# Kernel tuning notes

Measured on AMD Instinct MI355X. Metric: run time of the kernel, lower is better.

Reference implementation:

```python
import jax, jax.numpy as jnp
import numpy as np

N = 50000
E = 800000
D_IN, D_HID, D_OUT = 256, 256, 128


def _xavier(key, shape):
    fan_in, fan_out = shape
    limit = float(np.sqrt(6.0 / (fan_in + fan_out)))
    return jax.random.uniform(key, shape, jnp.float32, -limit, limit)


def setup_inputs() -> dict:
    key = jax.random.key(0)
    ks = jax.random.split(key, 12)
    x = jax.random.normal(ks[0], (N, D_IN), jnp.float32)
    edge_index = jax.random.randint(ks[1], (2, E), 0, N, dtype=jnp.int64)
    batch = jnp.zeros((N,), jnp.int64)
    # per-layer: message weight W, linear weight LW (stored [in, out]), bias b
    w1 = _xavier(ks[2], (D_IN, D_HID))
    lw1 = _xavier(ks[3], (D_IN, D_HID))
    lb1 = jnp.zeros((D_HID,), jnp.float32)
    w2 = _xavier(ks[4], (D_HID, D_HID))
    lw2 = _xavier(ks[5], (D_HID, D_HID))
    lb2 = jnp.zeros((D_HID,), jnp.float32)
    w3 = _xavier(ks[6], (D_HID, D_OUT))
    lw3 = _xavier(ks[7], (D_HID, D_OUT))
    lb3 = jnp.zeros((D_OUT,), jnp.float32)
    return {"x": x, "edge_index": edge_index, "batch": batch,
            "w1": w1, "lw1": lw1, "lb1": lb1,
            "w2": w2, "lw2": lw2, "lb2": lb2,
            "w3": w3, "lw3": lw3, "lb3": lb3}


def _gcn_layer(x, W, LW, b, row, col, norm):
    # message: norm * (x_j @ W); equivalent and cheaper: transform nodes once, gather
    xw = x @ W                                   # [N, out]
    msg = norm[:, None] * xw[row]                # [E, out]
    agg = jax.ops.segment_sum(msg, col, num_segments=x.shape[0])  # scatter-add at col
    return agg + x @ LW + b                      # residual linear path


def reference(x, edge_index, batch, w1, lw1, lb1, w2, lw2, lb2, w3, lw3, lb3):
    row, col = edge_index[0], edge_index[1]
    ones = jnp.ones((row.shape[0],), x.dtype)
    out_deg = jax.ops.segment_sum(ones, row, num_segments=N)
    in_deg = jax.ops.segment_sum(ones, col, num_segments=N)
    # inf at zero-degree nodes never gets gathered (those nodes have no edges)
    norm = out_deg[row] ** -0.5 * in_deg[col] ** -0.5  # [E]

    h = jax.nn.relu(_gcn_layer(x, w1, lw1, lb1, row, col, norm))
    h = jax.nn.relu(_gcn_layer(h, w2, lw2, lb2, row, col, norm))
    h = jax.nn.sigmoid(_gcn_layer(h, w3, lw3, lb3, row, col, norm))
    return h
```

## Files before the change

kernel.cpp:

```cpp
#include <hip/hip_runtime.h>
#include <hip/hip_bf16.h>
#include <math.h>

#define NNODES 50000
#define NEDGES 800000
#define HNB 128
#define HBINS 50176
#define SCAN_NB 196

typedef short s8v __attribute__((ext_vector_type(8)));
typedef float f4v __attribute__((ext_vector_type(4)));
using bf16 = __hip_bfloat16;

static __device__ __forceinline__ float bflo(unsigned int x) {
    union { unsigned int i; float f; } c; c.i = x << 16; return c.f;
}
static __device__ __forceinline__ float bfhi(unsigned int x) {
    union { unsigned int i; float f; } c; c.i = x & 0xffff0000u; return c.f;
}

static __device__ __forceinline__ void gload16(const void* g, void* l) {
    __builtin_amdgcn_global_load_lds(
        (const __attribute__((address_space(1))) unsigned int*)g,
        (__attribute__((address_space(3))) unsigned int*)l, 16, 0, 0);
}


__global__ void k_packbt(const float* __restrict__ W, const float* __restrict__ LW,
                         bf16* __restrict__ out, int K, int C) {
    int i = blockIdx.x * blockDim.x + threadIdx.x;
    int C2 = 2 * C;
    if (i >= K * C2) return;
    int n = i / K, k = i % K;
    float v = (n < C) ? W[k * C + n] : LW[k * C + (n - C)];
    out[i] = __float2bfloat16(v);
}


__global__ __launch_bounds__(256) void k_hist(const int* __restrict__ ei, ushort* __restrict__ partials) {
    __shared__ unsigned int h32[HBINS / 2];
    int b = blockIdx.x, row = blockIdx.y, t = threadIdx.x;
    for (int i = t; i < HBINS / 2; i += 256) h32[i] = 0;
    __syncthreads();
    const int chunk = NEDGES / HNB;
    int beg = b * chunk, end = beg + chunk;
    const int* p = ei + (size_t)row * NEDGES;
    for (int e = beg + t; e < end; e += 256) {
        int id = p[e];
        atomicAdd(&h32[id >> 1], 1u << (16 * (id & 1)));
    }
    __syncthreads();
    unsigned int* o32 = (unsigned int*)(partials + ((size_t)row * HNB + b) * HBINS);
    for (int i = t; i < HBINS / 2; i += 256) o32[i] = h32[i];
}

__global__ __launch_bounds__(256) void k_hist_reduce(const ushort* __restrict__ partials,
                                                     float* __restrict__ rsqrt_out,
                                                     int* __restrict__ in_cnt,
                                                     int* __restrict__ block_sums) {
    __shared__ int sm[256];
    int row = blockIdx.y;
    int i = blockIdx.x * 256 + threadIdx.x;
    const ushort* p = partials + (size_t)row * HNB * HBINS + i;
    int s = 0;
#pragma unroll 4
    for (int b = 0; b < HNB; ++b) s += p[(size_t)b * HBINS];
    if (row == 0) {
        if (i < NNODES) rsqrt_out[i] = rsqrtf((float)s);
    } else {
        if (i < NNODES) in_cnt[i] = s;
        sm[threadIdx.x] = s;
        __syncthreads();
        for (int off = 128; off > 0; off >>= 1) {
            if (threadIdx.x < off) sm[threadIdx.x] += sm[threadIdx.x + off];
            __syncthreads();
        }
        if (threadIdx.x == 0) block_sums[blockIdx.x] = sm[0];
    }
}


__global__ void k_scan_blocks(const int* __restrict__ block_sums, int* __restrict__ block_base, int nb) {
    __shared__ int s[256];
    int t = threadIdx.x;
    int v = (t < nb) ? block_sums[t] : 0;
    s[t] = v;
    __syncthreads();
    for (int off = 1; off < 256; off <<= 1) {
        int u = (t >= off) ? s[t - off] : 0;
        __syncthreads();
        s[t] += u;
        __syncthreads();
    }
    block_base[t] = s[t] - v;
}

__global__ void k_scan_final(const int* __restrict__ in_cnt, const int* __restrict__ block_base,
                             int* __restrict__ offsets, int* __restrict__ cursor) {
    __shared__ int s[256];
    int b = blockIdx.x, t = threadIdx.x;
    int i = b * 256 + t;
    int v = (i < NNODES) ? in_cnt[i] : 0;
    s[t] = v;
    __syncthreads();
    for (int off = 1; off < 256; off <<= 1) {
        int u = (t >= off) ? s[t - off] : 0;
        __syncthreads();
        s[t] += u;
        __syncthreads();
    }
    int excl = s[t] - v + block_base[b];
    if (i < NNODES) { offsets[i] = excl; cursor[i] = excl; }
    if (i == NNODES - 1) offsets[NNODES] = excl + v;
}

__global__ void k_scatter(const int* __restrict__ ei, int* __restrict__ cursor,
                          int* __restrict__ src_sorted) {
    int e = blockIdx.x * blockDim.x + threadIdx.x;
    if (e < NEDGES) {
        int r = ei[e], c = ei[NEDGES + e];
        int p = atomicAdd(&cursor[c], 1);
        src_sorted[p] = r;
    }
}

template<int D, int C2, int ACT>
__global__ __launch_bounds__(64) void k_agg_fused(const bf16* __restrict__ xwcat,
                                                  const int* __restrict__ offsets,
                                                  const int* __restrict__ src_sorted,
                                                  const float* __restrict__ rsqrt_out,
                                                  const float* __restrict__ bias,
                                                  void* __restrict__ out) {
    const int L = D / 8;
    const int G = 64 / L;
    const int U = 4;
    int lane = threadIdx.x;
    int v = blockIdx.x;
    int g = lane / L, sl = lane % L;

    int beg = offsets[v], end = offsets[v + 1];
    int deg = end - beg;
    int dcap = min(deg, 64);

    int id = 0; float wl = 0.f;
    if (lane < dcap) {
        id = src_sorted[beg + lane];
        wl = rsqrt_out[id];
    }

    float acc[U][8];
#pragma unroll
    for (int u = 0; u < U; ++u)
#pragma unroll
        for (int c = 0; c < 8; ++c) acc[u][c] = 0.f;

    const ushort* base = (const ushort*)xwcat + sl * 8;

    for (int e0 = 0; e0 < dcap; e0 += G * U) {
#pragma unroll
        for (int u = 0; u < U; ++u) {
            int e = e0 + u * G + g;
            int s = __shfl(id, e & 63, 64);
            float w = __shfl(wl, e & 63, 64);
            if (e >= dcap) w = 0.f;
            uint4 q = *(const uint4*)(base + (size_t)s * C2);
            acc[u][0] += w * bflo(q.x); acc[u][1] += w * bfhi(q.x);
            acc[u][2] += w * bflo(q.y); acc[u][3] += w * bfhi(q.y);
            acc[u][4] += w * bflo(q.z); acc[u][5] += w * bfhi(q.z);
            acc[u][6] += w * bflo(q.w); acc[u][7] += w * bfhi(q.w);
        }
    }
    for (int j = beg + 64 + g; j < end; j += G) {
        int s = src_sorted[j];
        float w = rsqrt_out[s];
        uint4 q = *(const uint4*)(base + (size_t)s * C2);
        acc[0][0] += w * bflo(q.x); acc[0][1] += w * bfhi(q.x);
        acc[0][2] += w * bflo(q.y); acc[0][3] += w * bfhi(q.y);
        acc[0][4] += w * bflo(q.z); acc[0][5] += w * bfhi(q.z);
        acc[0][6] += w * bflo(q.w); acc[0][7] += w * bfhi(q.w);
    }

#pragma unroll
    for (int c = 0; c < 8; ++c) acc[0][c] = (acc[0][c] + acc[1][c]) + (acc[2][c] + acc[3][c]);
#pragma unroll
    for (int d = 32; d >= L; d >>= 1) {
#pragma unroll
        for (int c = 0; c < 8; ++c) acc[0][c] += __shfl_down(acc[0][c], d, 64);
    }

    if (lane < L) {
        float sc = (deg > 0) ? rsqrtf((float)deg) : 0.f;
        const ushort* lwp = (const ushort*)xwcat + (size_t)v * C2 + D + sl * 8;
        uint4 ql = *(const uint4*)lwp;
        const float* bp = bias + sl * 8;
        float4 b0 = *(const float4*)bp, b1 = *(const float4*)(bp + 4);
        float h[8];
        h[0] = acc[0][0] * sc + bflo(ql.x) + b0.x;
        h[1] = acc[0][1] * sc + bfhi(ql.x) + b0.y;
        h[2] = acc[0][2] * sc + bflo(ql.y) + b0.z;
        h[3] = acc[0][3] * sc + bfhi(ql.y) + b0.w;
        h[4] = acc[0][4] * sc + bflo(ql.z) + b1.x;
        h[5] = acc[0][5] * sc + bfhi(ql.z) + b1.y;
        h[6] = acc[0][6] * sc + bflo(ql.w) + b1.z;
        h[7] = acc[0][7] * sc + bfhi(ql.w) + b1.w;
        if (ACT == 1) {
            union { bf16 hh[8]; uint4 u; } o;
#pragma unroll
            for (int c = 0; c < 8; ++c) o.hh[c] = __float2bfloat16(fmaxf(h[c], 0.f));
            *(uint4*)((ushort*)out + (size_t)v * D + sl * 8) = o.u;
        } else {
            float r[8];
#pragma unroll
            for (int c = 0; c < 8; ++c) r[c] = 1.f / (1.f + expf(-h[c]));
            float* op = (float*)out + (size_t)v * D + sl * 8;
            *(float4*)op = (float4){r[0], r[1], r[2], r[3]};
            *(float4*)(op + 4) = (float4){r[4], r[5], r[6], r[7]};
        }
    }
}

template<int C2, bool A_BF16>
__global__ __launch_bounds__(256) void k_gemm2(const void* __restrict__ Aptr,
                                               const bf16* __restrict__ BT,
                                               bf16* __restrict__ Out) {
    constexpr int R = NNODES;
    constexpr int GX = (NNODES + 127) / 128;
    constexpr int GY = C2 / 128;
    constexpr int NWG = GX * GY;
    __shared__ bf16 As[128 * 32];
    __shared__ bf16 Bs[128 * 32];

    int o = blockIdx.x;
    constexpr int qq = NWG / 8, rr = NWG % 8;
    int xcd = o & 7, idx = o >> 3;
    int lt = (xcd < rr ? xcd * (qq + 1) : rr * (qq + 1) + (xcd - rr) * qq) + idx;
    int r0 = (lt / GY) * 128;
    int n0 = (lt % GY) * 128;

    int t = threadIdx.x;
    int wave = t >> 6, lane = t & 63;
    int wr = wave >> 1, wc = wave & 1;

    f4v acc[4][4];
#pragma unroll
    for (int mi = 0; mi < 4; ++mi)
#pragma unroll
        for (int ni = 0; ni < 4; ++ni) acc[mi][ni] = (f4v){0.f, 0.f, 0.f, 0.f};

    int sr = t >> 2;
    int sk = (t & 3) * 8;
    int fr = t >> 1, fs = (t & 1) * 16;

    for (int k0 = 0; k0 < 256; k0 += 32) {
        if (A_BF16) {
            const bf16* Ab = (const bf16*)Aptr;
            gload16(Ab + (size_t)min(r0 + sr, R - 1) * 256 + k0 + sk,
                    (char*)As + wave * 1024);
            gload16(Ab + (size_t)min(r0 + sr + 64, R - 1) * 256 + k0 + sk,
                    (char*)As + 4096 + wave * 1024);
        } else {
            const float* Af = (const float*)Aptr + (size_t)min(r0 + fr, R - 1) * 256 + k0 + fs;
            float4 f0 = ((const float4*)Af)[0];
            float4 f1 = ((const float4*)Af)[1];
            float4 f2 = ((const float4*)Af)[2];
            float4 f3 = ((const float4*)Af)[3];
            union { bf16 h[16]; uint4 u[2]; } cv;
            cv.h[0]  = __float2bfloat16(f0.x); cv.h[1]  = __float2bfloat16(f0.y);
            cv.h[2]  = __float2bfloat16(f0.z); cv.h[3]  = __float2bfloat16(f0.w);
            cv.h[4]  = __float2bfloat16(f1.x); cv.h[5]  = __float2bfloat16(f1.y);
            cv.h[6]  = __float2bfloat16(f1.z); cv.h[7]  = __float2bfloat16(f1.w);
            cv.h[8]  = __float2bfloat16(f2.x); cv.h[9]  = __float2bfloat16(f2.y);
            cv.h[10] = __float2bfloat16(f2.z); cv.h[11] = __float2bfloat16(f2.w);
            cv.h[12] = __float2bfloat16(f3.x); cv.h[13] = __float2bfloat16(f3.y);
            cv.h[14] = __float2bfloat16(f3.z); cv.h[15] = __float2bfloat16(f3.w);
            *(uint4*)&As[fr * 32 + fs]     = cv.u[0];
            *(uint4*)&As[fr * 32 + fs + 8] = cv.u[1];
        }
        gload16(BT + (size_t)(n0 + sr) * 256 + k0 + sk,
                (char*)Bs + wave * 1024);
        gload16(BT + (size_t)(n0 + sr + 64) * 256 + k0 + sk,
                (char*)Bs + 4096 + wave * 1024);
        __syncthreads();

        int lr = lane & 15, lk = (lane >> 4) * 8;
        s8v a[4], b[4];
#pragma unroll
        for (int mi = 0; mi < 4; ++mi)
            a[mi] = *(const s8v*)&As[(wr * 64 + mi * 16 + lr) * 32 + lk];
#pragma unroll
        for (int ni = 0; ni < 4; ++ni)
            b[ni] = *(const s8v*)&Bs[(wc * 64 + ni * 16 + lr) * 32 + lk];
#pragma unroll
        for (int mi = 0; mi < 4; ++mi)
#pragma unroll
            for (int ni = 0; ni < 4; ++ni)
                acc[mi][ni] = __builtin_amdgcn_mfma_f32_16x16x32_bf16(a[mi], b[ni], acc[mi][ni], 0, 0, 0);
        __syncthreads();
    }

    int lr = lane & 15, lq = (lane >> 4) * 4;
#pragma unroll
    for (int mi = 0; mi < 4; ++mi) {
#pragma unroll
        for (int rj = 0; rj < 4; ++rj) {
            int grow = r0 + wr * 64 + mi * 16 + lq + rj;
            if (grow < R) {
#pragma unroll
                for (int ni = 0; ni < 4; ++ni) {
                    Out[(size_t)grow * C2 + n0 + wc * 64 + ni * 16 + lr] =
                        __float2bfloat16(acc[mi][ni][rj]);
                }
            }
        }
    }
}


extern "C" void kernel_launch(void* const* d_in, const int* in_sizes, int n_in,
                              void* d_out, int out_size, void* d_ws, size_t ws_size,
                              hipStream_t stream) {
    const float* x   = (const float*)d_in[0];
    const int*   ei  = (const int*)d_in[1];
    const float* w1  = (const float*)d_in[3];
    const float* lw1 = (const float*)d_in[4];
    const float* lb1 = (const float*)d_in[5];
    const float* w2  = (const float*)d_in[6];
    const float* lw2 = (const float*)d_in[7];
    const float* lb2 = (const float*)d_in[8];
    const float* w3  = (const float*)d_in[9];
    const float* lw3 = (const float*)d_in[10];
    const float* lb3 = (const float*)d_in[11];
    float* out = (float*)d_out;

    char* ws = (char*)d_ws;
    size_t off = 0;
    auto alloc = [&](size_t bytes) -> void* {
        void* p = ws + off;
        off += (bytes + 255) & ~(size_t)255;
        return p;
    };
    int*    in_cnt     = (int*)alloc((size_t)HBINS * 4);
    float*  rsqrt_out  = (float*)alloc((size_t)HBINS * 4);
    int*    offsets    = (int*)alloc((size_t)(NNODES + 1) * 4);
    int*    cursor     = (int*)alloc((size_t)NNODES * 4);
    int*    block_sums = (int*)alloc((size_t)256 * 4);
    int*    block_base = (int*)alloc((size_t)256 * 4);
    ushort* partials   = (ushort*)alloc((size_t)2 * HNB * HBINS * 2);
    int*    src_sorted = (int*)alloc((size_t)NEDGES * 4);
    bf16*   wcat1      = (bf16*)alloc((size_t)256 * 512 * 2);
    bf16*   wcat2      = (bf16*)alloc((size_t)256 * 512 * 2);
    bf16*   wcat3      = (bf16*)alloc((size_t)256 * 256 * 2);
    bf16*   xwcat      = (bf16*)alloc((size_t)NNODES * 512 * 2);
    bf16*   h1         = (bf16*)alloc((size_t)NNODES * 256 * 2);
    bf16*   h2         = (bf16*)alloc((size_t)NNODES * 256 * 2);

    k_packbt<<<512, 256, 0, stream>>>(w1, lw1, wcat1, 256, 256);
    k_packbt<<<512, 256, 0, stream>>>(w2, lw2, wcat2, 256, 256);
    k_packbt<<<256, 256, 0, stream>>>(w3, lw3, wcat3, 256, 128);

    k_hist<<<dim3(HNB, 2), 256, 0, stream>>>(ei, partials);
    k_hist_reduce<<<dim3(SCAN_NB, 2), 256, 0, stream>>>(partials, rsqrt_out, in_cnt, block_sums);
    k_scan_blocks<<<1, 256, 0, stream>>>(block_sums, block_base, SCAN_NB);
    k_scan_final<<<SCAN_NB, 256, 0, stream>>>(in_cnt, block_base, offsets, cursor);
    int eblocks = (NEDGES + 255) / 256;
    k_scatter<<<eblocks, 256, 0, stream>>>(ei, cursor, src_sorted);

    k_gemm2<512, false><<<391 * 4, 256, 0, stream>>>(x, wcat1, xwcat);
    k_agg_fused<256, 512, 1><<<NNODES, 64, 0, stream>>>(xwcat, offsets, src_sorted, rsqrt_out, lb1, h1);
    k_gemm2<512, true><<<391 * 4, 256, 0, stream>>>(h1, wcat2, xwcat);
    k_agg_fused<256, 512, 1><<<NNODES, 64, 0, stream>>>(xwcat, offsets, src_sorted, rsqrt_out, lb2, h2);
    k_gemm2<256, true><<<391 * 2, 256, 0, stream>>>(h2, wcat3, xwcat);
    k_agg_fused<128, 256, 2><<<NNODES, 64, 0, stream>>>(xwcat, offsets, src_sorted, rsqrt_out, lb3, out);
}
```

Before: 430.3 us.

## Replace atomic CSR scatter with rank-based placement and merge weight packing kernels

The histogram kernel now records each edge's local rank within its block from the shared-memory atomic's return value. The reduce kernel turns the per-block partial counts into exclusive prefix offsets in place. The scatter then computes each edge's final position directly, with no global atomics on a cursor array. The three weight-pack launches are merged into one, and the histogram block count is halved. This removes global atomic contention and a few launches, at the cost of an extra 1.6MB rank buffer and a serial per-node prefix loop over blocks.

Result: faster. 401.3 us (-6.7%).

```diff
diff --git a/kernel.cpp b/kernel.cpp
--- a/kernel.cpp
+++ b/kernel.cpp
@@ -4,7 +4,8 @@
 
 #define NNODES 50000
 #define NEDGES 800000
-#define HNB 128
+#define HNB 64
+#define HCHUNK (NEDGES / HNB)
 #define HBINS 50176
 #define SCAN_NB 196
 
@@ -26,50 +27,75 @@
 }
 
 
-__global__ void k_packbt(const float* __restrict__ W, const float* __restrict__ LW,
-                         bf16* __restrict__ out, int K, int C) {
-    int i = blockIdx.x * blockDim.x + threadIdx.x;
-    int C2 = 2 * C;
-    if (i >= K * C2) return;
-    int n = i / K, k = i % K;
+#define M1 (256 * 512)
+#define M2 (256 * 512)
+#define M3 (256 * 256)
+
+__global__ __launch_bounds__(256) void k_packall(
+        const float* __restrict__ w1, const float* __restrict__ lw1,
+        const float* __restrict__ w2, const float* __restrict__ lw2,
+        const float* __restrict__ w3, const float* __restrict__ lw3,
+        bf16* __restrict__ o1, bf16* __restrict__ o2, bf16* __restrict__ o3) {
+    int i = blockIdx.x * 256 + threadIdx.x;
+    const float* W; const float* LW; bf16* O; int C; int j;
+    if (i < M1)            { W = w1; LW = lw1; O = o1; C = 256; j = i; }
+    else if (i < M1 + M2)  { W = w2; LW = lw2; O = o2; C = 256; j = i - M1; }
+    else                   { W = w3; LW = lw3; O = o3; C = 128; j = i - M1 - M2; }
+    int n = j >> 8, k = j & 255;
     float v = (n < C) ? W[k * C + n] : LW[k * C + (n - C)];
-    out[i] = __float2bfloat16(v);
-}
-
-
-__global__ __launch_bounds__(256) void k_hist(const int* __restrict__ ei, ushort* __restrict__ partials) {
+    O[j] = __float2bfloat16(v);
+}
+
+
+__global__ __launch_bounds__(256) void k_hist(const int* __restrict__ ei,
+                                              ushort* __restrict__ partials,
+                                              ushort* __restrict__ lrank) {
     __shared__ unsigned int h32[HBINS / 2];
     int b = blockIdx.x, row = blockIdx.y, t = threadIdx.x;
     for (int i = t; i < HBINS / 2; i += 256) h32[i] = 0;
     __syncthreads();
-    const int chunk = NEDGES / HNB;
-    int beg = b * chunk, end = beg + chunk;
+    int beg = b * HCHUNK, end = beg + HCHUNK;
     const int* p = ei + (size_t)row * NEDGES;
-    for (int e = beg + t; e < end; e += 256) {
-        int id = p[e];
-        atomicAdd(&h32[id >> 1], 1u << (16 * (id & 1)));
+    if (row == 0) {
+        for (int e = beg + t; e < end; e += 256) {
+            int id = p[e];
+            atomicAdd(&h32[id >> 1], 1u << (16 * (id & 1)));
+        }
+    } else {
+        for (int e = beg + t; e < end; e += 256) {
+            int id = p[e];
+            unsigned int old = atomicAdd(&h32[id >> 1], 1u << (16 * (id & 1)));
+            lrank[e] = (ushort)((old >> (16 * (id & 1))) & 0xffffu);
+        }
     }
     __syncthreads();
     unsigned int* o32 = (unsigned int*)(partials + ((size_t)row * HNB + b) * HBINS);
     for (int i = t; i < HBINS / 2; i += 256) o32[i] = h32[i];
 }
 
-__global__ __launch_bounds__(256) void k_hist_reduce(const ushort* __restrict__ partials,
+__global__ __launch_bounds__(256) void k_hist_reduce(ushort* __restrict__ partials,
                                                      float* __restrict__ rsqrt_out,
                                                      int* __restrict__ in_cnt,
                                                      int* __restrict__ block_sums) {
     __shared__ int sm[256];
     int row = blockIdx.y;
     int i = blockIdx.x * 256 + threadIdx.x;
-    const ushort* p = partials + (size_t)row * HNB * HBINS + i;
-    int s = 0;
+    if (row == 0) {
+        const ushort* p = partials + i;
+        int s = 0;
 #pragma unroll 4
-    for (int b = 0; b < HNB; ++b) s += p[(size_t)b * HBINS];
-    if (row == 0) {
+        for (int b = 0; b < HNB; ++b) s += p[(size_t)b * HBINS];
         if (i < NNODES) rsqrt_out[i] = rsqrtf((float)s);
     } else {
-        if (i < NNODES) in_cnt[i] = s;
-        sm[threadIdx.x] = s;
+        ushort* p = partials + (size_t)HNB * HBINS + i;
+        int run = 0;
+        for (int b = 0; b < HNB; ++b) {
+            int c = p[(size_t)b * HBINS];
+            p[(size_t)b * HBINS] = (ushort)run;
+            run += c;
+        }
+        if (i < NNODES) in_cnt[i] = run;
+        sm[threadIdx.x] = (i < NNODES) ? run : 0;
         __syncthreads();
         for (int off = 128; off > 0; off >>= 1) {
             if (threadIdx.x < off) sm[threadIdx.x] += sm[threadIdx.x + off];
@@ -96,7 +122,7 @@
 }
 
 __global__ void k_scan_final(const int* __restrict__ in_cnt, const int* __restrict__ block_base,
-                             int* __restrict__ offsets, int* __restrict__ cursor) {
+                             int* __restrict__ offsets) {
     __shared__ int s[256];
     int b = blockIdx.x, t = threadIdx.x;
     int i = b * 256 + t;
@@ -110,17 +136,21 @@
         __syncthreads();
     }
     int excl = s[t] - v + block_base[b];
-    if (i < NNODES) { offsets[i] = excl; cursor[i] = excl; }
+    if (i < NNODES) offsets[i] = excl;
     if (i == NNODES - 1) offsets[NNODES] = excl + v;
 }
 
-__global__ void k_scatter(const int* __restrict__ ei, int* __restrict__ cursor,
-                          int* __restrict__ src_sorted) {
-    int e = blockIdx.x * blockDim.x + threadIdx.x;
+__global__ __launch_bounds__(256) void k_scatter_free(const int* __restrict__ ei,
+                                                      const int* __restrict__ offsets,
+                                                      const ushort* __restrict__ partials,
+                                                      const ushort* __restrict__ lrank,
+                                                      int* __restrict__ src_sorted) {
+    int e = blockIdx.x * 256 + threadIdx.x;
     if (e < NEDGES) {
         int r = ei[e], c = ei[NEDGES + e];
-        int p = atomicAdd(&cursor[c], 1);
-        src_sorted[p] = r;
+        int b = e / HCHUNK;
+        int pos = offsets[c] + (int)partials[(size_t)(HNB + b) * HBINS + c] + (int)lrank[e];
+        src_sorted[pos] = r;
     }
 }
 
@@ -342,10 +372,10 @@
     int*    in_cnt     = (int*)alloc((size_t)HBINS * 4);
     float*  rsqrt_out  = (float*)alloc((size_t)HBINS * 4);
     int*    offsets    = (int*)alloc((size_t)(NNODES + 1) * 4);
-    int*    cursor     = (int*)alloc((size_t)NNODES * 4);
     int*    block_sums = (int*)alloc((size_t)256 * 4);
     int*    block_base = (int*)alloc((size_t)256 * 4);
     ushort* partials   = (ushort*)alloc((size_t)2 * HNB * HBINS * 2);
+    ushort* lrank      = (ushort*)alloc((size_t)NEDGES * 2);
     int*    src_sorted = (int*)alloc((size_t)NEDGES * 4);
     bf16*   wcat1      = (bf16*)alloc((size_t)256 * 512 * 2);
     bf16*   wcat2      = (bf16*)alloc((size_t)256 * 512 * 2);
@@ -354,16 +384,15 @@
     bf16*   h1         = (bf16*)alloc((size_t)NNODES * 256 * 2);
     bf16*   h2         = (bf16*)alloc((size_t)NNODES * 256 * 2);
 
-    k_packbt<<<512, 256, 0, stream>>>(w1, lw1, wcat1, 256, 256);
-    k_packbt<<<512, 256, 0, stream>>>(w2, lw2, wcat2, 256, 256);
-    k_packbt<<<256, 256, 0, stream>>>(w3, lw3, wcat3, 256, 128);
-
-    k_hist<<<dim3(HNB, 2), 256, 0, stream>>>(ei, partials);
+    k_packall<<<(M1 + M2 + M3) / 256, 256, 0, stream>>>(
+        w1, lw1, w2, lw2, w3, lw3, wcat1, wcat2, wcat3);
+
+    k_hist<<<dim3(HNB, 2), 256, 0, stream>>>(ei, partials, lrank);
     k_hist_reduce<<<dim3(SCAN_NB, 2), 256, 0, stream>>>(partials, rsqrt_out, in_cnt, block_sums);
     k_scan_blocks<<<1, 256, 0, stream>>>(block_sums, block_base, SCAN_NB);
-    k_scan_final<<<SCAN_NB, 256, 0, stream>>>(in_cnt, block_base, offsets, cursor);
+    k_scan_final<<<SCAN_NB, 256, 0, stream>>>(in_cnt, block_base, offsets);
     int eblocks = (NEDGES + 255) / 256;
-    k_scatter<<<eblocks, 256, 0, stream>>>(ei, cursor, src_sorted);
+    k_scatter_free<<<eblocks, 256, 0, stream>>>(ei, offsets, partials, lrank, src_sorted);
 
     k_gemm2<512, false><<<391 * 4, 256, 0, stream>>>(x, wcat1, xwcat);
     k_agg_fused<256, 512, 1><<<NNODES, 64, 0, stream>>>(xwcat, offsets, src_sorted, rsqrt_out, lb1, h1);
```
